# Kernel optimization log

Hardware: AMD Instinct MI355X
Metric: run time of the kernel (lower is better)

## Reference

```python
import jax, jax.numpy as jnp
import numpy as np

LEVEL_SHAPES = [(100, 134), (50, 67), (25, 34), (13, 17)]  # (H, W) per feature level
NH, NL, NP, D, DFF = 8, 4, 4, 256, 1024
DH = D // NH
LTOT = sum(h * w for h, w in LEVEL_SHAPES)  # 17821
BS, NQ = 4, 300


def _ln(x, w, b):
    m = x.mean(-1, keepdims=True)
    v = ((x - m) ** 2).mean(-1, keepdims=True)
    return (x - m) / jnp.sqrt(v + 1e-5) * w + b


def _mha(q, k, v, in_w, in_b, out_w, out_b):
    B, N, _ = q.shape
    wq, wk, wv = jnp.split(in_w, 3, axis=0)
    bq, bk, bv = jnp.split(in_b, 3)
    qh = (q @ wq.T + bq).reshape(B, N, NH, DH)
    kh = (k @ wk.T + bk).reshape(B, N, NH, DH)
    vh = (v @ wv.T + bv).reshape(B, N, NH, DH)
    a = jax.nn.softmax(jnp.einsum('bqhd,bkhd->bhqk', qh, kh) / float(np.sqrt(DH)), axis=-1)
    o = jnp.einsum('bhqk,bkhd->bqhd', a, vh).reshape(B, N, D)
    return o @ out_w.T + out_b


def _bilinear(img, grid):
    # img [B,C,H,W]; grid [B,N,2] in [-1,1]; align_corners=False, zero padding
    B, C, H, W = img.shape
    x = (grid[..., 0] + 1.0) * 0.5 * W - 0.5
    y = (grid[..., 1] + 1.0) * 0.5 * H - 0.5
    x0f = jnp.floor(x); y0f = jnp.floor(y)
    wx = x - x0f; wy = y - y0f
    x0 = x0f.astype(jnp.int32); y0 = y0f.astype(jnp.int32)
    flat = img.reshape(B, C, H * W)

    def gather(xi, yi):
        m = ((xi >= 0) & (xi < W) & (yi >= 0) & (yi < H)).astype(img.dtype)
        idx = jnp.clip(yi, 0, H - 1) * W + jnp.clip(xi, 0, W - 1)
        g = jnp.take_along_axis(flat, jnp.broadcast_to(idx[:, None, :], (B, C, idx.shape[-1])), axis=2)
        return g * m[:, None, :]

    return (gather(x0, y0) * ((1 - wx) * (1 - wy))[:, None]
            + gather(x0 + 1, y0) * (wx * (1 - wy))[:, None]
            + gather(x0, y0 + 1) * ((1 - wx) * wy)[:, None]
            + gather(x0 + 1, y0 + 1) * (wx * wy)[:, None])


def _msdeform(value, loc, aw):
    # value [B,L,NH,DH]; loc [B,Nq,NH,NL,NP,2] in [0,1]; aw [B,Nq,NH,NL,NP]
    B, Nq = loc.shape[0], loc.shape[1]
    outs = []
    start = 0
    for l, (Hl, Wl) in enumerate(LEVEL_SHAPES):
        v = value[:, start:start + Hl * Wl].transpose(0, 2, 3, 1).reshape(B * NH, DH, Hl, Wl)
        g = (2.0 * loc[:, :, :, l] - 1.0).transpose(0, 2, 1, 3, 4).reshape(B * NH, Nq * NP, 2)
        outs.append(_bilinear(v, g).reshape(B * NH, DH, Nq, NP))
        start += Hl * Wl
    samp = jnp.stack(outs, axis=3)  # [B*NH, DH, Nq, NL, NP]
    w = aw.transpose(0, 2, 1, 3, 4).reshape(B * NH, 1, Nq, NL, NP)
    out = (samp * w).sum(axis=(3, 4))  # [B*NH, DH, Nq]
    return out.reshape(B, NH, DH, Nq).transpose(0, 3, 1, 2).reshape(B, Nq, D)


def _deform_branch(q, ref, src_other, vw, vb, ow, ob, aww, awb, outw, outb):
    B, Nq, _ = q.shape
    value = (src_other @ vw.T + vb).reshape(B, -1, NH, DH)
    off = (q @ ow.T + ob).reshape(B, Nq, NH, NL, NP, 2)
    aw = jax.nn.softmax((q @ aww.T + awb).reshape(B, Nq, NH, NL * NP), axis=-1).reshape(B, Nq, NH, NL, NP)
    norm = jnp.array([[w, h] for h, w in LEVEL_SHAPES], dtype=q.dtype)  # (W,H) per level
    loc = ref[:, :, None, :, None, :] + off / norm[None, None, None, :, None, :]
    return _msdeform(value, loc, aw) @ outw.T + outb


def reference(tgt_RGB, tgt_T, query_pos_RGB, query_pos_T, ref_RGB, ref_T, src_RGB, src_T,
              sa_in_w, sa_in_b, sa_out_w, sa_out_b, ln_w, ln_b,
              ffn_w1, ffn_b1, ffn_w2, ffn_b2,
              val_w, val_b, off_w, off_b, aw_w, aw_b, cout_w, cout_b):
    # --- dual self-attention (eval mode: dropout = identity) ---
    q_RGB = tgt_RGB + query_pos_RGB
    q_T = tgt_T + query_pos_T
    sa_RGB = _mha(q_RGB, q_RGB, tgt_RGB, sa_in_w[0], sa_in_b[0], sa_out_w[0], sa_out_b[0])
    sa_T = _mha(q_T, q_T, tgt_T, sa_in_w[1], sa_in_b[1], sa_out_w[1], sa_out_b[1])
    tgt_RGB = _ln(tgt_RGB + sa_RGB, ln_w[0, 1], ln_b[0, 1])  # norm2_RGB
    tgt_T = _ln(tgt_T + sa_T, ln_w[1, 1], ln_b[1, 1])        # norm2_T
    # --- interactive multi-scale deformable cross-attn: RGB queries sample T memory & vice versa ---
    qc_RGB = tgt_RGB + query_pos_RGB
    qc_T = tgt_T + query_pos_T
    t2_RGB = _deform_branch(qc_RGB, ref_RGB, src_T, val_w[0], val_b[0], off_w[0], off_b[0], aw_w[0], aw_b[0], cout_w[0], cout_b[0])
    t2_T = _deform_branch(qc_T, ref_T, src_RGB, val_w[1], val_b[1], off_w[1], off_b[1], aw_w[1], aw_b[1], cout_w[1], cout_b[1])
    F_RGB, F_T = t2_RGB, t2_T
    # cross residuals exactly as in the torch layer (note the modality swap)
    r = tgt_T + t2_RGB
    t = r + t2_T
    tgt_RGB = _ln(r, ln_w[0, 0], ln_b[0, 0])  # norm1_RGB
    tgt_T = _ln(t, ln_w[1, 0], ln_b[1, 0])    # norm1_T
    # --- FFNs ---
    tgt_RGB = _ln(tgt_RGB + (jax.nn.relu(tgt_RGB @ ffn_w1[0].T + ffn_b1[0]) @ ffn_w2[0].T + ffn_b2[0]), ln_w[0, 2], ln_b[0, 2])
    tgt_T = _ln(tgt_T + (jax.nn.relu(tgt_T @ ffn_w1[1].T + ffn_b1[1]) @ ffn_w2[1].T + ffn_b2[1]), ln_w[1, 2], ln_b[1, 2])
    return tgt_RGB, tgt_T, F_RGB, F_T


def setup_inputs() -> dict:
    key = jax.random.key(0)
    ks = jax.random.split(key, 24)
    s = 0.05
    w = lambda k, shp: jax.random.normal(k, shp, dtype=jnp.float32) * s
    return {
        'tgt_RGB': jax.random.normal(ks[0], (BS, NQ, D), jnp.float32),
        'tgt_T': jax.random.normal(ks[1], (BS, NQ, D), jnp.float32),
        'query_pos_RGB': jax.random.normal(ks[2], (BS, NQ, D), jnp.float32),
        'query_pos_T': jax.random.normal(ks[3], (BS, NQ, D), jnp.float32),
        'ref_RGB': jax.random.uniform(ks[4], (BS, NQ, NL, 2), jnp.float32),
        'ref_T': jax.random.uniform(ks[5], (BS, NQ, NL, 2), jnp.float32),
        'src_RGB': jax.random.normal(ks[6], (BS, LTOT, D), jnp.float32),
        'src_T': jax.random.normal(ks[7], (BS, LTOT, D), jnp.float32),
        'sa_in_w': w(ks[8], (2, 3 * D, D)),
        'sa_in_b': jnp.zeros((2, 3 * D), jnp.float32),
        'sa_out_w': w(ks[9], (2, D, D)),
        'sa_out_b': jnp.zeros((2, D), jnp.float32),
        'ln_w': jnp.ones((2, 3, D), jnp.float32),
        'ln_b': jnp.zeros((2, 3, D), jnp.float32),
        'ffn_w1': w(ks[10], (2, DFF, D)),
        'ffn_b1': jnp.zeros((2, DFF), jnp.float32),
        'ffn_w2': w(ks[11], (2, D, DFF)),
        'ffn_b2': jnp.zeros((2, D), jnp.float32),
        'val_w': w(ks[12], (2, D, D)),
        'val_b': jnp.zeros((2, D), jnp.float32),
        'off_w': w(ks[13], (2, NH * NL * NP * 2, D)),
        'off_b': jax.random.normal(ks[14], (2, NH * NL * NP * 2), jnp.float32) * 0.5,
        'aw_w': w(ks[15], (2, NH * NL * NP, D)),
        'aw_b': jnp.zeros((2, NH * NL * NP), jnp.float32),
        'cout_w': w(ks[16], (2, D, D)),
        'cout_b': jnp.zeros((2, D), jnp.float32),
    }
```

## Files before the change

kernel.cpp:

```cpp
#include <hip/hip_runtime.h>
#include <cstddef>
#include <math.h>

#define NTOK 1200
#define LTOT_C 17821
#define MVAL 71284
#define STOK (NTOK * 256)

typedef __attribute__((ext_vector_type(8))) short bhalf8;
typedef __attribute__((ext_vector_type(4))) float f32x4;

static __device__ __forceinline__ short f2bf(float f) {
    unsigned u = __builtin_bit_cast(unsigned, f);
    u += 0x7fffu + ((u >> 16) & 1u);
    return (short)(u >> 16);
}
static __device__ __forceinline__ float bf2f(short s) {
    unsigned u = ((unsigned)(unsigned short)s) << 16;
    return __builtin_bit_cast(float, u);
}
static __device__ __forceinline__ bhalf8 cvt8(float4 a, float4 b) {
    bhalf8 h;
    h[0] = f2bf(a.x); h[1] = f2bf(a.y); h[2] = f2bf(a.z); h[3] = f2bf(a.w);
    h[4] = f2bf(b.x); h[5] = f2bf(b.y); h[6] = f2bf(b.z); h[7] = f2bf(b.w);
    return h;
}

struct WcvtArgs { const float* s[10]; short* d[10]; int n[10]; };
__global__ __launch_bounds__(256) void wcvt(WcvtArgs a) {
    const int ti = blockIdx.y;
    const float* s = a.s[ti];
    short* d = a.d[ti];
    const int n = a.n[ti];
    for (int base = (blockIdx.x * 256 + threadIdx.x) * 8; base < n; base += gridDim.x * 256 * 8) {
        const float4 f0 = *reinterpret_cast<const float4*>(s + base);
        const float4 f1 = *reinterpret_cast<const float4*>(s + base + 4);
        *reinterpret_cast<bhalf8*>(d + base) = cvt8(f0, f1);
    }
}

__global__ __launch_bounds__(256) void prep_act(
    const float* __restrict__ tgt0, const float* __restrict__ tgt1,
    const float* __restrict__ pos0, const float* __restrict__ pos1,
    short* __restrict__ qb_bf, short* __restrict__ tgtb,
    const float* __restrict__ off_b, const float* __restrict__ aw_b,
    float* __restrict__ baw)
{
    const int z = blockIdx.y;
    if (blockIdx.x == 0 && z == 0) {
        for (int i = threadIdx.x; i < 768; i += 256) {
            const int zz = i / 384, j = i - zz * 384;
            baw[i] = (j < 256) ? off_b[zz * 256 + j] : aw_b[zz * 128 + (j - 256)];
        }
    }
    const float* tg = z ? tgt1 : tgt0;
    const float* ps = z ? pos1 : pos0;
    const int base = (blockIdx.x * 256 + threadIdx.x) * 8;
    if (base >= STOK) return;
    const float4 t0 = *reinterpret_cast<const float4*>(tg + base);
    const float4 t1 = *reinterpret_cast<const float4*>(tg + base + 4);
    const float4 p0 = *reinterpret_cast<const float4*>(ps + base);
    const float4 p1 = *reinterpret_cast<const float4*>(ps + base + 4);
    float4 s0 = make_float4(t0.x + p0.x, t0.y + p0.y, t0.z + p0.z, t0.w + p0.w);
    float4 s1 = make_float4(t1.x + p1.x, t1.y + p1.y, t1.z + p1.z, t1.w + p1.w);
    *reinterpret_cast<bhalf8*>(qb_bf + (size_t)z * STOK + base) = cvt8(s0, s1);
    *reinterpret_cast<bhalf8*>(tgtb + (size_t)z * STOK + base) = cvt8(t0, t1);
}

template<bool A_FP32, bool HASRES, bool RELU, bool OUT_BF16, int BM, int NK>
__global__ __launch_bounds__(256) void gemm_bf16(
    const void* __restrict__ Av, const void* __restrict__ Av1, size_t aStrideZ, int lda,
    const short* __restrict__ Wv, size_t wStrideZ, int ldw,
    const float* __restrict__ bias, size_t biasStrideZ,
    const float* __restrict__ Res0, const float* __restrict__ Res1, int ldr,
    void* __restrict__ Cv, size_t cStrideZ, int ldc,
    int M)
{
    constexpr int AIT = BM / 32;
    constexpr int MFR = BM / 32;
    __shared__ short As[BM * 64];
    __shared__ short Bs[128 * 64];
    const int z = blockIdx.z;
    const void* Asel = (Av1 != nullptr && z == 1) ? Av1 : Av;
    const size_t zoff = (Av1 != nullptr) ? 0 : (size_t)z * aStrideZ;
    const short* W = Wv + (size_t)z * wStrideZ;
    const float* bz = bias + (size_t)z * biasStrideZ;
    const int t = threadIdx.x;
    const int wave = t >> 6, lane = t & 63;
    const int l15 = lane & 15, l4 = lane >> 4;
    const int wr = wave >> 1, wc = wave & 1;
    const int bm = blockIdx.y * BM, bn = blockIdx.x * 128;
    f32x4 acc[MFR][4] = {};

    float4 paf[2][AIT][2];
    bhalf8 pab[2][AIT];
    bhalf8 pwb[2][4];

    auto issue = [&](int slot, int k0) {
        #pragma unroll
        for (int i = 0; i < AIT; ++i) {
            const int G = t + i * 256;
            const int m = G >> 3, g = G & 7;
            const int row = bm + m;
            if (A_FP32) {
                if (row < M) {
                    const float* s = (const float*)Asel + zoff + (size_t)row * lda + k0 + g * 8;
                    paf[slot][i][0] = *reinterpret_cast<const float4*>(s);
                    paf[slot][i][1] = *reinterpret_cast<const float4*>(s + 4);
                } else {
                    paf[slot][i][0] = make_float4(0.f, 0.f, 0.f, 0.f);
                    paf[slot][i][1] = make_float4(0.f, 0.f, 0.f, 0.f);
                }
            } else {
                if (row < M) {
                    pab[slot][i] = *reinterpret_cast<const bhalf8*>(
                        (const short*)Asel + zoff + (size_t)row * lda + k0 + g * 8);
                } else {
                    #pragma unroll
                    for (int q = 0; q < 8; ++q) pab[slot][i][q] = 0;
                }
            }
        }
        #pragma unroll
        for (int i = 0; i < 4; ++i) {
            const int G = t + i * 256;
            const int n = G >> 3, g = G & 7;
            pwb[slot][i] = *reinterpret_cast<const bhalf8*>(W + (size_t)(bn + n) * ldw + k0 + g * 8);
        }
    };
    auto commit = [&](int slot) {
        #pragma unroll
        for (int i = 0; i < AIT; ++i) {
            const int G = t + i * 256;
            const int m = G >> 3, g = G & 7;
            bhalf8 h;
            if (A_FP32) h = cvt8(paf[slot][i][0], paf[slot][i][1]);
            else h = pab[slot][i];
            *reinterpret_cast<bhalf8*>(&As[m * 64 + ((g ^ (m & 7)) << 3)]) = h;
        }
        #pragma unroll
        for (int i = 0; i < 4; ++i) {
            const int G = t + i * 256;
            const int n = G >> 3, g = G & 7;
            *reinterpret_cast<bhalf8*>(&Bs[n * 64 + ((g ^ (n & 7)) << 3)]) = pwb[slot][i];
        }
    };
    auto compute = [&]() {
        #pragma unroll
        for (int kf = 0; kf < 2; ++kf) {
            bhalf8 af[MFR], bfv[4];
            #pragma unroll
            for (int mf = 0; mf < MFR; ++mf) {
                const int m = wr * (BM / 2) + (mf << 4) + l15;
                const int g = ((kf << 2) + l4) ^ (m & 7);
                af[mf] = *reinterpret_cast<const bhalf8*>(&As[m * 64 + (g << 3)]);
            }
            #pragma unroll
            for (int nf = 0; nf < 4; ++nf) {
                const int n = (wc << 6) + (nf << 4) + l15;
                const int g = ((kf << 2) + l4) ^ (n & 7);
                bfv[nf] = *reinterpret_cast<const bhalf8*>(&Bs[n * 64 + (g << 3)]);
            }
            #pragma unroll
            for (int mf = 0; mf < MFR; ++mf)
                #pragma unroll
                for (int nf = 0; nf < 4; ++nf)
                    acc[mf][nf] = __builtin_amdgcn_mfma_f32_16x16x32_bf16(
                        af[mf], bfv[nf], acc[mf][nf], 0, 0, 0);
        }
    };

    issue(0, 0);
    issue(1, 64);
    __builtin_amdgcn_sched_barrier(0);
    commit(0);
    #pragma unroll
    for (int ks = 0; ks < NK; ++ks) {
        __syncthreads();
        if (ks + 2 < NK) issue(ks & 1, (ks + 2) << 6);
        __builtin_amdgcn_sched_barrier(0);
        compute();
        __syncthreads();
        if (ks + 1 < NK) commit((ks + 1) & 1);
    }

    const float* Rz = HASRES ? (z ? Res1 : Res0) : nullptr;
    float br[4];
    #pragma unroll
    for (int nf = 0; nf < 4; ++nf) br[nf] = bz[bn + (wc << 6) + (nf << 4) + l15];
    #pragma unroll
    for (int mf = 0; mf < MFR; ++mf) {
        #pragma unroll
        for (int j = 0; j < 4; ++j) {
            const int row = bm + wr * (BM / 2) + (mf << 4) + (l4 << 2) + j;
            if (row >= M) continue;
            const int colbase = bn + (wc << 6);
            #pragma unroll
            for (int nf = 0; nf < 4; ++nf) {
                const int col = colbase + (nf << 4) + l15;
                float v = acc[mf][nf][j] + br[nf];
                if (HASRES) v += Rz[(size_t)row * ldr + col];
                if (RELU) v = fmaxf(v, 0.f);
                if (OUT_BF16)
                    ((short*)Cv + (size_t)z * cStrideZ)[(size_t)row * ldc + col] = f2bf(v);
                else
                    ((float*)Cv + (size_t)z * cStrideZ)[(size_t)row * ldc + col] = v;
            }
        }
    }
}

__global__ __launch_bounds__(256) void attn2_kernel(
    const float* __restrict__ qkv_base, short* __restrict__ out_base)
{
    const float scale = 0.17677669529663687f;
    const float* qkv = qkv_base + (size_t)blockIdx.z * 921600;
    short* outp = out_base + (size_t)blockIdx.z * STOK;
    const int b = blockIdx.y >> 3, h = blockIdx.y & 7;
    const int t = threadIdx.x;
    const int ql = t & 31;
    const int kg = t >> 5;
    const int q = blockIdx.x * 32 + ql;
    const bool act = q < 300;
    const float* base = qkv + (size_t)b * 300 * 768;

    float qreg[32];
    if (act) {
        const float4* qp = reinterpret_cast<const float4*>(base + (size_t)q * 768 + h * 32);
        #pragma unroll
        for (int d4 = 0; d4 < 8; ++d4) {
            const float4 v = qp[d4];
            qreg[d4 * 4 + 0] = v.x; qreg[d4 * 4 + 1] = v.y;
            qreg[d4 * 4 + 2] = v.z; qreg[d4 * 4 + 3] = v.w;
        }
    }
    __shared__ float Ks[64][32];
    __shared__ float Vs[64][32];
    float m = -1e30f, l = 0.f, o[32];
    #pragma unroll
    for (int d = 0; d < 32; ++d) o[d] = 0.f;

    for (int k0 = 0; k0 < 300; k0 += 64) {
        const int cnt = min(64, 300 - k0);
        __syncthreads();
        for (int i = t; i < cnt * 32; i += 256) {
            const int kr = i >> 5, d = i & 31;
            Ks[kr][d] = base[(size_t)(k0 + kr) * 768 + 256 + h * 32 + d];
            Vs[kr][d] = base[(size_t)(k0 + kr) * 768 + 512 + h * 32 + d];
        }
        __syncthreads();
        if (act) {
            for (int kk = kg; kk < cnt; kk += 8) {
                const float4* krow = reinterpret_cast<const float4*>(&Ks[kk][0]);
                float s = 0.f;
                #pragma unroll
                for (int d4 = 0; d4 < 8; ++d4) {
                    const float4 kv = krow[d4];
                    s += qreg[d4 * 4 + 0] * kv.x + qreg[d4 * 4 + 1] * kv.y
                       + qreg[d4 * 4 + 2] * kv.z + qreg[d4 * 4 + 3] * kv.w;
                }
                s *= scale;
                const float4* vrow = reinterpret_cast<const float4*>(&Vs[kk][0]);
                if (s <= m) {
                    const float e = __expf(s - m);
                    l += e;
                    #pragma unroll
                    for (int d4 = 0; d4 < 8; ++d4) {
                        const float4 vv = vrow[d4];
                        o[d4 * 4 + 0] += e * vv.x; o[d4 * 4 + 1] += e * vv.y;
                        o[d4 * 4 + 2] += e * vv.z; o[d4 * 4 + 3] += e * vv.w;
                    }
                } else {
                    const float c = __expf(m - s);
                    l = l * c + 1.f;
                    #pragma unroll
                    for (int d4 = 0; d4 < 8; ++d4) {
                        const float4 vv = vrow[d4];
                        o[d4 * 4 + 0] = o[d4 * 4 + 0] * c + vv.x;
                        o[d4 * 4 + 1] = o[d4 * 4 + 1] * c + vv.y;
                        o[d4 * 4 + 2] = o[d4 * 4 + 2] * c + vv.z;
                        o[d4 * 4 + 3] = o[d4 * 4 + 3] * c + vv.w;
                    }
                    m = s;
                }
            }
        }
    }
    __shared__ float pm[32][8];
    __shared__ float pl[32][8];
    __shared__ float po[8][32][33];
    pm[ql][kg] = m; pl[ql][kg] = l;
    #pragma unroll
    for (int d = 0; d < 32; ++d) po[kg][d][ql] = o[d];
    __syncthreads();
    if (kg == 0) {
        float M = pm[ql][0];
        #pragma unroll
        for (int i = 1; i < 8; ++i) M = fmaxf(M, pm[ql][i]);
        float L = 0.f;
        #pragma unroll
        for (int i = 0; i < 8; ++i) L += pl[ql][i] * __expf(pm[ql][i] - M);
        const float invL = 1.f / L;
        #pragma unroll
        for (int i = 0; i < 8; ++i) pm[ql][i] = __expf(pm[ql][i] - M) * invL;
    }
    __syncthreads();
    if (act) {
        #pragma unroll
        for (int dd = 0; dd < 4; ++dd) {
            const int d = kg * 4 + dd;
            float v = 0.f;
            #pragma unroll
            for (int i = 0; i < 8; ++i) v += pm[ql][i] * po[i][d][ql];
            outp[((size_t)b * 300 + q) * 256 + h * 32 + d] = f2bf(v);
        }
    }
}

#define LN_BODY(vexpr, widx)                                                  \
    const int row = blockIdx.x, t = threadIdx.x, z = blockIdx.y;              \
    (void)z;                                                                  \
    const int i = row * 256 + t;                                              \
    const float v = (vexpr);                                                  \
    __shared__ float r1[4], r2[4];                                            \
    float s = v;                                                              \
    _Pragma("unroll")                                                         \
    for (int o = 32; o; o >>= 1) s += __shfl_xor(s, o);                       \
    if ((t & 63) == 0) r1[t >> 6] = s;                                        \
    __syncthreads();                                                          \
    const float mean = (r1[0] + r1[1] + r1[2] + r1[3]) * (1.f / 256.f);       \
    const float dd = v - mean;                                                \
    float sq = dd * dd;                                                       \
    _Pragma("unroll")                                                         \
    for (int o = 32; o; o >>= 1) sq += __shfl_xor(sq, o);                     \
    if ((t & 63) == 0) r2[t >> 6] = sq;                                       \
    __syncthreads();                                                          \
    const float var = (r2[0] + r2[1] + r2[2] + r2[3]) * (1.f / 256.f);        \
    const float y = dd * rsqrtf(var + 1e-5f) * ln_w[(widx) * 256 + t]         \
                    + ln_b[(widx) * 256 + t];

__global__ __launch_bounds__(256) void ln2_fused(
    const float* __restrict__ presum, const float* __restrict__ pos0,
    const float* __restrict__ pos1, const float* __restrict__ ln_w,
    const float* __restrict__ ln_b, short* __restrict__ qc_bf,
    float* __restrict__ tgt2T)
{
    LN_BODY(presum[(size_t)z * STOK + i], z * 3 + 1)
    const float* pos = z ? pos1 : pos0;
    qc_bf[(size_t)z * STOK + i] = f2bf(y + pos[i]);
    if (z == 1) tgt2T[i] = y;
}

__global__ __launch_bounds__(256) void ln1_fused(
    const float* __restrict__ tgt2T, const float* __restrict__ out2,
    const float* __restrict__ out3, const float* __restrict__ ln_w,
    const float* __restrict__ ln_b, short* __restrict__ ln1b,
    float* __restrict__ ln1f)
{
    LN_BODY(tgt2T[row * 256 + t] + out2[row * 256 + t] + (z ? out3[row * 256 + t] : 0.f), z * 3 + 0)
    ln1b[(size_t)z * STOK + i] = f2bf(y);
    ln1f[(size_t)z * STOK + i] = y;
}

__global__ __launch_bounds__(256) void ln3_kernel(
    const float* __restrict__ ffny, const float* __restrict__ ln_w,
    const float* __restrict__ ln_b, float* __restrict__ o0,
    float* __restrict__ o1)
{
    LN_BODY(ffny[(size_t)z * STOK + i], z * 3 + 2)
    (z ? o1 : o0)[i] = y;
}

__global__ __launch_bounds__(256) void sample_kernel(
    const short* __restrict__ valb, const float* __restrict__ oaw,
    const float* __restrict__ ref0, const float* __restrict__ ref1,
    short* __restrict__ out)
{
    const int HL[4] = {100, 50, 25, 13};
    const int WL[4] = {134, 67, 34, 17};
    const int ST[4] = {0, 13400, 16750, 17600};
    const int z = blockIdx.y;
    const int t = threadIdx.x;
    const int wave = t >> 6, lane = t & 63;
    const int qi = wave >> 1, hh = wave & 1;
    const int pp = lane >> 5, h4 = (lane >> 3) & 3, dl = lane & 7;
    const int h = hh * 4 + h4;
    const int bq = blockIdx.x * 2 + qi;
    const int b = bq / 300;
    const float* op = oaw + ((size_t)z * NTOK + bq) * 384;
    const float* offp = op + h * 32;
    const float* awp  = op + 256 + h * 16;
    const float* refp = (z ? ref1 : ref0) + (size_t)bq * 8;
    const short* vb = valb + (size_t)z * MVAL * 256 + (size_t)b * LTOT_C * 256;
    const int co = h * 32 + dl * 4;

    float w16[16];
    float mx = -1e30f;
    #pragma unroll
    for (int i = 0; i < 16; ++i) { w16[i] = awp[i]; mx = fmaxf(mx, w16[i]); }
    float ssum = 0.f;
    #pragma unroll
    for (int i = 0; i < 16; ++i) { w16[i] = __expf(w16[i] - mx); ssum += w16[i]; }
    const float sinv = 1.f / ssum;

    float a0 = 0.f, a1 = 0.f, a2 = 0.f, a3 = 0.f;
#define TAP(cond, ridx, wv)                                                   \
    if (cond) {                                                               \
        const short4 sv = *reinterpret_cast<const short4*>(                   \
            vb + (size_t)(ridx) * 256 + co);                                  \
        a0 += (wv) * bf2f(sv.x); a1 += (wv) * bf2f(sv.y);                     \
        a2 += (wv) * bf2f(sv.z); a3 += (wv) * bf2f(sv.w);                     \
    }
    #pragma unroll
    for (int l = 0; l < 4; ++l) {
        const int Wl = WL[l], Hl = HL[l];
        const float rx = refp[l * 2] * (float)Wl - 0.5f;
        const float ry = refp[l * 2 + 1] * (float)Hl - 0.5f;
        #pragma unroll
        for (int j = 0; j < 2; ++j) {
            const int p = pp * 2 + j;
            const float px = rx + offp[(l * 4 + p) * 2];
            const float py = ry + offp[(l * 4 + p) * 2 + 1];
            const float wgt = w16[l * 4 + p] * sinv;
            const float x0f = floorf(px), y0f = floorf(py);
            const float wx = px - x0f, wy = py - y0f;
            const int x0 = (int)x0f, y0 = (int)y0f;
            const bool xa = (x0 >= 0) & (x0 < Wl);
            const bool xb = (x0 >= -1) & (x0 < Wl - 1);
            const bool ya = (y0 >= 0) & (y0 < Hl);
            const bool yb = (y0 >= -1) & (y0 < Hl - 1);
            const int rbase = ST[l] + y0 * Wl + x0;
            const float w00 = wgt * (1.f - wx) * (1.f - wy);
            const float w10 = wgt * wx * (1.f - wy);
            const float w01 = wgt * (1.f - wx) * wy;
            const float w11 = wgt * wx * wy;
            TAP(ya & xa, rbase, w00)
            TAP(ya & xb, rbase + 1, w10)
            TAP(yb & xa, rbase + Wl, w01)
            TAP(yb & xb, rbase + Wl + 1, w11)
        }
    }
#undef TAP
    a0 += __shfl_xor(a0, 32);
    a1 += __shfl_xor(a1, 32);
    a2 += __shfl_xor(a2, 32);
    a3 += __shfl_xor(a3, 32);
    if (pp == 0) {
        short4 o;
        o.x = f2bf(a0); o.y = f2bf(a1); o.z = f2bf(a2); o.w = f2bf(a3);
        *reinterpret_cast<short4*>(&out[((size_t)z * NTOK + bq) * 256 + co]) = o;
    }
}

extern "C" void kernel_launch(void* const* d_in, const int* in_sizes, int n_in,
                              void* d_out, int out_size, void* d_ws, size_t ws_size,
                              hipStream_t stream) {
    const float* tgt[2] = {(const float*)d_in[0], (const float*)d_in[1]};
    const float* pos[2] = {(const float*)d_in[2], (const float*)d_in[3]};
    const float* ref[2] = {(const float*)d_in[4], (const float*)d_in[5]};
    const float* src[2] = {(const float*)d_in[6], (const float*)d_in[7]};
    const float* sa_in_w  = (const float*)d_in[8];
    const float* sa_in_b  = (const float*)d_in[9];
    const float* sa_out_w = (const float*)d_in[10];
    const float* sa_out_b = (const float*)d_in[11];
    const float* ln_w = (const float*)d_in[12];
    const float* ln_b = (const float*)d_in[13];
    const float* ffn_w1 = (const float*)d_in[14];
    const float* ffn_b1 = (const float*)d_in[15];
    const float* ffn_w2 = (const float*)d_in[16];
    const float* ffn_b2 = (const float*)d_in[17];
    const float* val_w = (const float*)d_in[18];
    const float* val_b = (const float*)d_in[19];
    const float* off_w = (const float*)d_in[20];
    const float* off_b = (const float*)d_in[21];
    const float* aw_w = (const float*)d_in[22];
    const float* aw_b = (const float*)d_in[23];
    const float* cout_w = (const float*)d_in[24];
    const float* cout_b = (const float*)d_in[25];

    char* base = (char*)d_ws;
    size_t off = 0;
    auto alloc = [&](size_t bytes) -> char* {
        char* p = base + off;
        off += (bytes + 255) & ~(size_t)255;
        return p;
    };
    short* wbf   = (short*)alloc((size_t)2031616 * 2);
    float* baw   = (float*)alloc(768 * 4);
    short* qb_bf = (short*)alloc((size_t)2 * STOK * 2);
    short* tgtb  = (short*)alloc((size_t)2 * STOK * 2);
    float* qkv   = (float*)alloc((size_t)2 * 921600 * 4);
    short* attno = (short*)alloc((size_t)2 * STOK * 2);
    float* presum= (float*)alloc((size_t)2 * STOK * 4);
    short* qc_bf = (short*)alloc((size_t)2 * STOK * 2);
    float* tgt2T = (float*)alloc((size_t)STOK * 4);
    float* oawb  = (float*)alloc((size_t)2 * NTOK * 384 * 4);
    short* valb  = (short*)alloc((size_t)2 * MVAL * 256 * 2);
    short* samp  = (short*)alloc((size_t)2 * STOK * 2);
    short* ln1b  = (short*)alloc((size_t)2 * STOK * 2);
    float* ln1f  = (float*)alloc((size_t)2 * STOK * 4);
    short* ffnh  = (short*)alloc((size_t)2 * NTOK * 1024 * 2);
    float* ffny  = (float*)alloc((size_t)2 * STOK * 4);

    short* sa_in_bf  = wbf + 0;
    short* sa_out_bf = wbf + 393216;
    short* ffn1_bf   = wbf + 524288;
    short* ffn2_bf   = wbf + 1048576;
    short* val_bf    = wbf + 1572864;
    short* cout_bf   = wbf + 1703936;
    short* oaw_bf    = wbf + 1835008;

    float* out0 = (float*)d_out;
    float* out1 = out0 + STOK;
    float* out2 = out1 + STOK;
    float* out3 = out2 + STOK;

    const dim3 b256(256);

    WcvtArgs wa;
    wa.s[0] = sa_in_w;        wa.d[0] = sa_in_bf;       wa.n[0] = 393216;
    wa.s[1] = sa_out_w;       wa.d[1] = sa_out_bf;      wa.n[1] = 131072;
    wa.s[2] = ffn_w1;         wa.d[2] = ffn1_bf;        wa.n[2] = 524288;
    wa.s[3] = ffn_w2;         wa.d[3] = ffn2_bf;        wa.n[3] = 524288;
    wa.s[4] = val_w;          wa.d[4] = val_bf;         wa.n[4] = 131072;
    wa.s[5] = cout_w;         wa.d[5] = cout_bf;        wa.n[5] = 131072;
    wa.s[6] = off_w;          wa.d[6] = oaw_bf;         wa.n[6] = 65536;
    wa.s[7] = aw_w;           wa.d[7] = oaw_bf + 65536; wa.n[7] = 32768;
    wa.s[8] = off_w + 65536;  wa.d[8] = oaw_bf + 98304; wa.n[8] = 65536;
    wa.s[9] = aw_w + 32768;   wa.d[9] = oaw_bf + 163840;wa.n[9] = 32768;
    wcvt<<<dim3(128, 10), b256, 0, stream>>>(wa);

    prep_act<<<dim3(150, 2), b256, 0, stream>>>(tgt[0], tgt[1], pos[0], pos[1],
                                                qb_bf, tgtb, off_b, aw_b, baw);

    gemm_bf16<true, false, false, true, 128, 4><<<dim3(2, 557, 2), b256, 0, stream>>>(
        src[1], src[0], 0, 256, val_bf, 65536, 256, val_b, 256, nullptr, nullptr, 0,
        valb, (size_t)MVAL * 256, 256, MVAL);

    gemm_bf16<false, false, false, false, 64, 4><<<dim3(4, 19, 2), b256, 0, stream>>>(
        qb_bf, nullptr, (size_t)STOK, 256, sa_in_bf, 196608, 256, sa_in_b, 768,
        nullptr, nullptr, 0, qkv, 921600, 768, NTOK);
    gemm_bf16<false, false, false, false, 64, 4><<<dim3(2, 19, 2), b256, 0, stream>>>(
        tgtb, nullptr, (size_t)STOK, 256, sa_in_bf + 512 * 256, 196608, 256, sa_in_b + 512, 768,
        nullptr, nullptr, 0, qkv + 512, 921600, 768, NTOK);

    attn2_kernel<<<dim3(10, 32, 2), b256, 0, stream>>>(qkv, attno);

    gemm_bf16<false, true, false, false, 64, 4><<<dim3(2, 19, 2), b256, 0, stream>>>(
        attno, nullptr, (size_t)STOK, 256, sa_out_bf, 65536, 256, sa_out_b, 256,
        tgt[0], tgt[1], 256, presum, (size_t)STOK, 256, NTOK);

    ln2_fused<<<dim3(NTOK, 2), b256, 0, stream>>>(presum, pos[0], pos[1], ln_w, ln_b, qc_bf, tgt2T);

    gemm_bf16<false, false, false, false, 64, 4><<<dim3(3, 19, 2), b256, 0, stream>>>(
        qc_bf, nullptr, (size_t)STOK, 256, oaw_bf, 98304, 256, baw, 384,
        nullptr, nullptr, 0, oawb, (size_t)NTOK * 384, 384, NTOK);

    sample_kernel<<<dim3(600, 2), b256, 0, stream>>>(valb, oawb, ref[0], ref[1], samp);

    gemm_bf16<false, false, false, false, 64, 4><<<dim3(2, 19, 2), b256, 0, stream>>>(
        samp, nullptr, (size_t)STOK, 256, cout_bf, 65536, 256, cout_b, 256,
        nullptr, nullptr, 0, out2, (size_t)STOK, 256, NTOK);

    ln1_fused<<<dim3(NTOK, 2), b256, 0, stream>>>(tgt2T, out2, out3, ln_w, ln_b, ln1b, ln1f);

    gemm_bf16<false, false, true, true, 64, 4><<<dim3(8, 19, 2), b256, 0, stream>>>(
        ln1b, nullptr, (size_t)STOK, 256, ffn1_bf, 262144, 256, ffn_b1, 1024,
        nullptr, nullptr, 0, ffnh, (size_t)NTOK * 1024, 1024, NTOK);

    gemm_bf16<false, true, false, false, 64, 16><<<dim3(2, 19, 2), b256, 0, stream>>>(
        ffnh, nullptr, (size_t)NTOK * 1024, 1024, ffn2_bf, 262144, 1024, ffn_b2, 256,
        ln1f, ln1f + STOK, 256, ffny, (size_t)STOK, 256, NTOK);

    ln3_kernel<<<dim3(NTOK, 2), b256, 0, stream>>>(ffny, ln_w, ln_b, out0, out1);
}
```

Baseline: 208.4 us.

## Stage GEMM tiles via direct global-to-LDS loads with double-buffered shared memory

Replaces the register-staged load/convert/commit pipeline in the bf16 GEMM with global_load_lds (buffer-to-LDS DMA) into double-buffered shared tiles, with the swizzle applied on the source address. FP32 A operands are now stored raw in LDS and converted to bf16 with packed conversions at fragment-read time. This aims to cut VGPR pressure and VALU/LDS-store instructions and to drop one barrier per k-step. In exchange it doubles LDS use, especially for FP32 A tiles, which may reduce occupancy, and it relies on a single barrier for correct async completion ordering.

```diff
diff --git a/kernel.cpp b/kernel.cpp
--- a/kernel.cpp
+++ b/kernel.cpp
@@ -1,4 +1,5 @@
 #include <hip/hip_runtime.h>
+#include <hip/hip_bf16.h>
 #include <cstddef>
 #include <math.h>
 
@@ -24,6 +25,19 @@
     h[0] = f2bf(a.x); h[1] = f2bf(a.y); h[2] = f2bf(a.z); h[3] = f2bf(a.w);
     h[4] = f2bf(b.x); h[5] = f2bf(b.y); h[6] = f2bf(b.z); h[7] = f2bf(b.w);
     return h;
+}
+static __device__ __forceinline__ bhalf8 cvt8pk(float4 a, float4 b) {
+    union { bhalf8 h; __hip_bfloat162 v[4]; } u;
+    u.v[0] = __float22bfloat162_rn(make_float2(a.x, a.y));
+    u.v[1] = __float22bfloat162_rn(make_float2(a.z, a.w));
+    u.v[2] = __float22bfloat162_rn(make_float2(b.x, b.y));
+    u.v[3] = __float22bfloat162_rn(make_float2(b.z, b.w));
+    return u.h;
+}
+static __device__ __forceinline__ void gload_lds16(const void* g, void* l) {
+    __builtin_amdgcn_global_load_lds(
+        (const __attribute__((address_space(1))) void*)g,
+        (__attribute__((address_space(3))) void*)l, 16, 0, 0);
 }
 
 struct WcvtArgs { const float* s[10]; short* d[10]; int n[10]; };
@@ -76,10 +90,12 @@
     void* __restrict__ Cv, size_t cStrideZ, int ldc,
     int M)
 {
-    constexpr int AIT = BM / 32;
     constexpr int MFR = BM / 32;
-    __shared__ short As[BM * 64];
-    __shared__ short Bs[128 * 64];
+    constexpr int ASH = BM * 64 * (A_FP32 ? 2 : 1);
+    constexpr int ACH = (ASH * 2) / 1024;
+    constexpr int ACW = ACH / 4;
+    __shared__ alignas(16) short As[2][ASH];
+    __shared__ alignas(16) short Bs[2][128 * 64];
     const int z = blockIdx.z;
     const void* Asel = (Av1 != nullptr && z == 1) ? Av1 : Av;
     const size_t zoff = (Av1 != nullptr) ? 0 : (size_t)z * aStrideZ;
@@ -92,60 +108,42 @@
     const int bm = blockIdx.y * BM, bn = blockIdx.x * 128;
     f32x4 acc[MFR][4] = {};
 
-    float4 paf[2][AIT][2];
-    bhalf8 pab[2][AIT];
-    bhalf8 pwb[2][4];
-
-    auto issue = [&](int slot, int k0) {
-        #pragma unroll
-        for (int i = 0; i < AIT; ++i) {
-            const int G = t + i * 256;
-            const int m = G >> 3, g = G & 7;
-            const int row = bm + m;
-            if (A_FP32) {
-                if (row < M) {
-                    const float* s = (const float*)Asel + zoff + (size_t)row * lda + k0 + g * 8;
-                    paf[slot][i][0] = *reinterpret_cast<const float4*>(s);
-                    paf[slot][i][1] = *reinterpret_cast<const float4*>(s + 4);
-                } else {
-                    paf[slot][i][0] = make_float4(0.f, 0.f, 0.f, 0.f);
-                    paf[slot][i][1] = make_float4(0.f, 0.f, 0.f, 0.f);
-                }
-            } else {
-                if (row < M) {
-                    pab[slot][i] = *reinterpret_cast<const bhalf8*>(
-                        (const short*)Asel + zoff + (size_t)row * lda + k0 + g * 8);
-                } else {
-                    #pragma unroll
-                    for (int q = 0; q < 8; ++q) pab[slot][i][q] = 0;
-                }
+    const int nr8 = lane >> 3, q8 = lane & 7;
+    auto stageW = [&](int k0, int buf) {
+        #pragma unroll
+        for (int i = 0; i < 4; ++i) {
+            const int c = wave * 4 + i;
+            const int n = c * 8 + nr8;
+            gload_lds16(W + (size_t)(bn + n) * ldw + k0 + ((q8 ^ nr8) << 3),
+                        (char*)&Bs[buf][0] + c * 1024);
+        }
+    };
+    const int mr4 = lane >> 4, q16 = lane & 15;
+    auto stageA = [&](int k0, int buf) {
+        if (A_FP32) {
+            #pragma unroll
+            for (int i = 0; i < ACW; ++i) {
+                const int c = wave * ACW + i;
+                const int m = c * 4 + mr4;
+                const int row = min(bm + m, M - 1);
+                const int p = q16 >> 1, h = q16 & 1;
+                const float* src = (const float*)Asel + zoff + (size_t)row * lda + k0
+                                   + (((p ^ (m & 7)) << 3) + (h << 2));
+                gload_lds16(src, (char*)&As[buf][0] + c * 1024);
             }
-        }
-        #pragma unroll
-        for (int i = 0; i < 4; ++i) {
-            const int G = t + i * 256;
-            const int n = G >> 3, g = G & 7;
-            pwb[slot][i] = *reinterpret_cast<const bhalf8*>(W + (size_t)(bn + n) * ldw + k0 + g * 8);
+        } else {
+            #pragma unroll
+            for (int i = 0; i < ACW; ++i) {
+                const int c = wave * ACW + i;
+                const int m = c * 8 + nr8;
+                const int row = min(bm + m, M - 1);
+                const short* src = (const short*)Asel + zoff + (size_t)row * lda + k0
+                                   + ((q8 ^ (m & 7)) << 3);
+                gload_lds16(src, (char*)&As[buf][0] + c * 1024);
+            }
         }
     };
-    auto commit = [&](int slot) {
-        #pragma unroll
-        for (int i = 0; i < AIT; ++i) {
-            const int G = t + i * 256;
-            const int m = G >> 3, g = G & 7;
-            bhalf8 h;
-            if (A_FP32) h = cvt8(paf[slot][i][0], paf[slot][i][1]);
-            else h = pab[slot][i];
-            *reinterpret_cast<bhalf8*>(&As[m * 64 + ((g ^ (m & 7)) << 3)]) = h;
-        }
-        #pragma unroll
-        for (int i = 0; i < 4; ++i) {
-            const int G = t + i * 256;
-            const int n = G >> 3, g = G & 7;
-            *reinterpret_cast<bhalf8*>(&Bs[n * 64 + ((g ^ (n & 7)) << 3)]) = pwb[slot][i];
-        }
-    };
-    auto compute = [&]() {
+    auto compute = [&](int buf) {
         #pragma unroll
         for (int kf = 0; kf < 2; ++kf) {
             bhalf8 af[MFR], bfv[4];
@@ -153,13 +151,20 @@
             for (int mf = 0; mf < MFR; ++mf) {
                 const int m = wr * (BM / 2) + (mf << 4) + l15;
                 const int g = ((kf << 2) + l4) ^ (m & 7);
-                af[mf] = *reinterpret_cast<const bhalf8*>(&As[m * 64 + (g << 3)]);
+                if (A_FP32) {
+                    const float* Af = (const float*)&As[buf][0];
+                    const float4 f0 = *reinterpret_cast<const float4*>(&Af[m * 64 + (g << 3)]);
+                    const float4 f1 = *reinterpret_cast<const float4*>(&Af[m * 64 + (g << 3) + 4]);
+                    af[mf] = cvt8pk(f0, f1);
+                } else {
+                    af[mf] = *reinterpret_cast<const bhalf8*>(&As[buf][m * 64 + (g << 3)]);
+                }
             }
             #pragma unroll
             for (int nf = 0; nf < 4; ++nf) {
                 const int n = (wc << 6) + (nf << 4) + l15;
                 const int g = ((kf << 2) + l4) ^ (n & 7);
-                bfv[nf] = *reinterpret_cast<const bhalf8*>(&Bs[n * 64 + (g << 3)]);
+                bfv[nf] = *reinterpret_cast<const bhalf8*>(&Bs[buf][n * 64 + (g << 3)]);
             }
             #pragma unroll
             for (int mf = 0; mf < MFR; ++mf)
@@ -170,18 +175,17 @@
         }
     };
 
-    issue(0, 0);
-    issue(1, 64);
-    __builtin_amdgcn_sched_barrier(0);
-    commit(0);
+    stageA(0, 0);
+    stageW(0, 0);
+    __syncthreads();
     #pragma unroll
     for (int ks = 0; ks < NK; ++ks) {
+        if (ks + 1 < NK) {
+            stageA((ks + 1) << 6, (ks + 1) & 1);
+            stageW((ks + 1) << 6, (ks + 1) & 1);
+        }
+        compute(ks & 1);
         __syncthreads();
-        if (ks + 2 < NK) issue(ks & 1, (ks + 2) << 6);
-        __builtin_amdgcn_sched_barrier(0);
-        compute();
-        __syncthreads();
-        if (ks + 1 < NK) commit((ks + 1) & 1);
     }
 
     const float* Rz = HASRES ? (z ? Res1 : Res0) : nullptr;
```

New measurement: 264.8 us. 1.27x slower.
